# Kernel tuning notes

Measured on AMD Instinct MI355X. Metric: run time of the kernel, lower is better.

The kernel has to match this reference:

```python
import jax, jax.numpy as jnp
import numpy as np

TEMPERATURE = 0.1
THR = 0.2
BORDER_RM = 2


def setup_inputs() -> dict:
    key = jax.random.key(0)
    k0, k1 = jax.random.split(key)
    N, L, S, C = 2, 4800, 4800, 256
    return {
        "feat_c0": jax.random.normal(k0, (N, L, C), dtype=jnp.float32),
        "feat_c1": jax.random.normal(k1, (N, S, C), dtype=jnp.float32),
        "h0c": 60, "w0c": 80, "h1c": 60, "w1c": 80,
    }


def _border_valid(h, w, bd):
    # Faithful to torch mask_border: only the FIRST `bd` rows/cols are masked
    # (the negative slices m[:, -bd:0] in the source are empty no-ops).
    vh = jnp.arange(h) >= bd
    vw = jnp.arange(w) >= bd
    return (vh[:, None] & vw[None, :]).reshape(-1)  # [h*w]


def reference(feat_c0, feat_c1, h0c, w0c, h1c, w1c):
    C = feat_c0.shape[-1]
    scale = 1.0 / (C ** 0.5)  # 'sqrt_feat_dim' feature normalizer
    f0 = feat_c0 * scale
    f1 = feat_c1 * scale

    # dual-softmax confidence matrix [N, L, S]
    sim = jnp.einsum("nlc,nsc->nls", f0, f1) / TEMPERATURE
    conf = jax.nn.softmax(sim, axis=1) * jax.nn.softmax(sim, axis=2)

    # threshold + border removal (no padding masks in data)
    mask = conf > THR
    valid0 = _border_valid(h0c, w0c, BORDER_RM)  # [L]
    valid1 = _border_valid(h1c, w1c, BORDER_RM)  # [S]
    mask = mask & valid0[None, :, None] & valid1[None, None, :]

    # mutual nearest neighbour filtering
    mask = mask & (conf == conf.max(axis=2, keepdims=True)) \
                & (conf == conf.max(axis=1, keepdims=True))

    # match extraction (JIT-friendly padded form):
    # j_ids[b, i] = column of the (unique) True in row i; match_mask marks valid rows.
    j_ids = jnp.argmax(mask, axis=2)               # [N, L] int
    match_mask = jnp.any(mask, axis=2)             # [N, L] bool
    mconf = jnp.take_along_axis(conf, j_ids[..., None], axis=2)[..., 0]
    mconf = jnp.where(match_mask, mconf, 0.0)      # [N, L]

    return conf, match_mask, j_ids, mconf
```

## Files before the change

### kernel.cpp

```cpp
#include <hip/hip_runtime.h>


#define Ncst 2
#define Lc 4800
#define Sc 4800
#define Cc 256
#define KA 512
#define KB 256
#define LP 4864
#define THRC 0.2f

typedef float f32x4 __attribute__((ext_vector_type(4)));
typedef _Float16 f16x8 __attribute__((ext_vector_type(8)));
typedef _Float16 f16x4 __attribute__((ext_vector_type(4)));

#define AS1(p) ((__attribute__((address_space(1))) void*)(p))
#define AS3(p) ((__attribute__((address_space(3))) void*)(p))

__global__ __launch_bounds__(256) void convert_kernel(
    const float* __restrict__ f0, const float* __restrict__ f1,
    unsigned short* __restrict__ A2, unsigned short* __restrict__ B2,
    float* __restrict__ rs, float* __restrict__ cs)
{
    int idx = blockIdx.x * 256 + threadIdx.x;
    if (idx < Ncst * Lc) { rs[idx] = 0.f; cs[idx] = 0.f; }
    if (idx >= Ncst * LP * (Cc / 8)) return;
    int k8  = idx & (Cc / 8 - 1);
    int row = (idx >> 5) % LP;
    int n   = idx / (LP * (Cc / 8));

    float av[8], bv[8];
    if (row < Lc) {
        const float4* pa = (const float4*)(f0 + ((size_t)n * Lc + row) * Cc + k8 * 8);
        float4 a0 = pa[0], a1 = pa[1];
        av[0]=a0.x; av[1]=a0.y; av[2]=a0.z; av[3]=a0.w;
        av[4]=a1.x; av[5]=a1.y; av[6]=a1.z; av[7]=a1.w;
        const float4* pb = (const float4*)(f1 + ((size_t)n * Sc + row) * Cc + k8 * 8);
        float4 b0 = pb[0], b1 = pb[1];
        bv[0]=b0.x; bv[1]=b0.y; bv[2]=b0.z; bv[3]=b0.w;
        bv[4]=b1.x; bv[5]=b1.y; bv[6]=b1.z; bv[7]=b1.w;
    } else {
        for (int i = 0; i < 8; ++i) { av[i] = 0.f; bv[i] = 0.f; }
    }

    _Float16 ahi[8], alo[8], bhi[8];
#pragma unroll
    for (int i = 0; i < 8; ++i) {
        _Float16 h = (_Float16)av[i];
        ahi[i] = h;
        alo[i] = (_Float16)(av[i] - (float)h);
        bhi[i] = (_Float16)bv[i];
    }
    size_t abase = ((size_t)n * LP + row) * KA + k8 * 8;
    size_t bbase = ((size_t)n * LP + row) * KB + k8 * 8;
    *(uint4*)&A2[abase]       = *(uint4*)ahi;
    *(uint4*)&A2[abase + 256] = *(uint4*)alo;
    *(uint4*)&B2[bbase]       = *(uint4*)bhi;
}

template <int DUMMY>
__global__ __launch_bounds__(256, 3) void gemm_kernel(
    const unsigned short* __restrict__ A2, const unsigned short* __restrict__ B2,
    _Float16* __restrict__ eout, float* __restrict__ rs, float* __restrict__ cs)
{
    __shared__ __attribute__((aligned(16))) unsigned short lds[2][1536 * 8];

    int flat = blockIdx.x + 38 * blockIdx.y + 1444 * blockIdx.z;
    int m    = (flat & 7) * 361 + (flat >> 3);
    const int tn = m % 38;
    const int tm = (m / 38) % 38;
    const int n  = m / 1444;

    const int tid  = threadIdx.x;
    const int wave = tid >> 6;
    const int lane = tid & 63;
    const int wm   = wave >> 1;
    const int wn   = wave & 1;
    const int ml   = lane & 15;
    const int kq   = lane >> 4;

    const unsigned short* Ab = A2 + ((size_t)n * LP + (size_t)tm * 128) * KA;
    const unsigned short* Bb = B2 + ((size_t)n * LP + (size_t)tn * 128) * KB;

    const unsigned short* gsrc[6];
    int gdst[6];
#pragma unroll
    for (int c = 0; c < 6; ++c) {
        int reg = c >> 1;
        int s   = (c & 1) * 256 + tid;
        int row = s >> 2;
        int q   = (s & 3) ^ ((row >> 1) & 3);
        if (reg == 0)      gsrc[c] = Ab + (size_t)row * KA + q * 8;
        else if (reg == 1) gsrc[c] = Ab + (size_t)row * KA + 256 + q * 8;
        else               gsrc[c] = Bb + (size_t)row * KB + q * 8;
        gdst[c] = (reg * 512 + s) * 8;
    }

    int aoff[4], boff[4];
#pragma unroll
    for (int i = 0; i < 4; ++i) {
        int ar = wm * 64 + i * 16 + ml;
        aoff[i] = (ar * 4 + (kq ^ ((ar >> 1) & 3))) * 8;
        int br = wn * 64 + i * 16 + ml;
        boff[i] = (br * 4 + (kq ^ ((br >> 1) & 3))) * 8;
    }

#define STAGE(bb, tt) do { _Pragma("unroll") for (int c_ = 0; c_ < 6; ++c_) \
    __builtin_amdgcn_global_load_lds(AS1(gsrc[c_] + (tt) * 32), AS3(&lds[bb][gdst[c_]]), 16, 0, 0); } while (0)

    f32x4 acc[4][4] = {};

    STAGE(0, 0);
    __syncthreads();

#pragma unroll
    for (int t = 0; t < 8; ++t) {
        const int b = t & 1;
        if (t < 7) STAGE(b ^ 1, t + 1);
        f16x8 ah[4], al[4], bf_[4];
#pragma unroll
        for (int i = 0; i < 4; ++i) {
            ah[i]  = *(const f16x8*)&lds[b][aoff[i]];
            al[i]  = *(const f16x8*)&lds[b][4096 + aoff[i]];
            bf_[i] = *(const f16x8*)&lds[b][8192 + boff[i]];
        }
#pragma unroll
        for (int i = 0; i < 4; ++i)
#pragma unroll
            for (int j = 0; j < 4; ++j) {
                acc[i][j] = __builtin_amdgcn_mfma_f32_16x16x32_f16(ah[i], bf_[j], acc[i][j], 0, 0, 0);
                acc[i][j] = __builtin_amdgcn_mfma_f32_16x16x32_f16(al[i], bf_[j], acc[i][j], 0, 0, 0);
            }
        __syncthreads();
    }
#undef STAGE

    const float alpha = 5.0f / 128.0f;
#pragma unroll
    for (int i = 0; i < 4; ++i)
#pragma unroll
        for (int r = 0; r < 4; ++r) {
            int gl = tm * 128 + wm * 64 + i * 16 + kq * 4 + r;
            bool rok = gl < Lc;
#pragma unroll
            for (int j = 0; j < 4; ++j) {
                int gs = tn * 128 + wn * 64 + j * 16 + ml;
                bool ok = rok && (gs < Sc);
                acc[i][j][r] = ok ? __expf(acc[i][j][r] * alpha) : 0.f;
            }
        }
#pragma unroll
    for (int i = 0; i < 4; ++i)
#pragma unroll
        for (int r = 0; r < 4; ++r) {
            float rp = acc[i][0][r] + acc[i][1][r] + acc[i][2][r] + acc[i][3][r];
            rp += __shfl_xor(rp, 1);
            rp += __shfl_xor(rp, 2);
            rp += __shfl_xor(rp, 4);
            rp += __shfl_xor(rp, 8);
            int gl = tm * 128 + wm * 64 + i * 16 + kq * 4 + r;
            if (ml == 0 && gl < Lc) atomicAdd(&rs[(size_t)n * Lc + gl], rp);
        }
#pragma unroll
    for (int j = 0; j < 4; ++j) {
        float cp = 0.f;
#pragma unroll
        for (int i = 0; i < 4; ++i)
#pragma unroll
            for (int r = 0; r < 4; ++r) cp += acc[i][j][r];
        cp += __shfl_xor(cp, 16);
        cp += __shfl_xor(cp, 32);
        int gs = tn * 128 + wn * 64 + j * 16 + ml;
        if (kq == 0 && gs < Sc) atomicAdd(&cs[(size_t)n * Sc + gs], cp);
    }

    float* tb = (float*)&lds[0][0];
    const int CS = 132;
#pragma unroll
    for (int p = 0; p < 2; ++p) {
        __syncthreads();
#pragma unroll
        for (int ih = 0; ih < 2; ++ih) {
            int i   = 2 * p + ih;
            int lr0 = wm * 32 + ih * 16 + kq * 4;
#pragma unroll
            for (int j = 0; j < 4; ++j) {
                int col = wn * 64 + j * 16 + ml;
#pragma unroll
                for (int r = 0; r < 4; ++r)
                    tb[(lr0 + r) * CS + col] = acc[i][j][r];
            }
        }
        __syncthreads();
#pragma unroll
        for (int u = 0; u < 8; ++u) {
            int idx = u * 256 + tid;
            int lr  = idx >> 5;
            int cv  = idx & 31;
            int grow = tm * 128 + (lr >> 5) * 64 + (2 * p + ((lr >> 4) & 1)) * 16 + (lr & 15);
            int gcol = tn * 128 + cv * 4;
            if (grow < Lc && gcol + 3 < Sc) {
                f32x4 v = *(const f32x4*)&tb[lr * CS + cv * 4];
                f16x4 h;
                h.x = (_Float16)v.x; h.y = (_Float16)v.y;
                h.z = (_Float16)v.z; h.w = (_Float16)v.w;
                *(f16x4*)&eout[((size_t)n * Lc + grow) * Sc + gcol] = h;
            }
        }
    }
}

__global__ __launch_bounds__(256) void conf_kernel(
    const _Float16* __restrict__ E, float* __restrict__ conf,
    const float* __restrict__ rs, const float* __restrict__ cs,
    float* __restrict__ rcm)
{
    __shared__ float sw[4];
    int b = blockIdx.x;
    int n = b / Lc;
    const f16x8* erow = (const f16x8*)(E + (size_t)b * Sc);
    f32x4* crow = (f32x4*)(conf + (size_t)b * Sc);
    const f32x4* csv = (const f32x4*)(cs + (size_t)n * Sc);
    int tid = threadIdx.x;
    float riv = 1.0f / rs[b];
    float lmax = 0.f;
    for (int v = tid; v < Sc / 8; v += 256) {
        f16x8 e8 = erow[v];
        f32x4 ca = csv[2 * v], cb = csv[2 * v + 1];
        f32x4 o0, o1;
        o0.x = (float)e8[0]; o0.y = (float)e8[1]; o0.z = (float)e8[2]; o0.w = (float)e8[3];
        o1.x = (float)e8[4]; o1.y = (float)e8[5]; o1.z = (float)e8[6]; o1.w = (float)e8[7];
        f32x4 ia, ib;
        ia.x = 1.0f / ca.x; ia.y = 1.0f / ca.y; ia.z = 1.0f / ca.z; ia.w = 1.0f / ca.w;
        ib.x = 1.0f / cb.x; ib.y = 1.0f / cb.y; ib.z = 1.0f / cb.z; ib.w = 1.0f / cb.w;
        o0 = o0 * o0 * riv * ia;
        o1 = o1 * o1 * riv * ib;
        __builtin_nontemporal_store(o0, &crow[2 * v]);
        __builtin_nontemporal_store(o1, &crow[2 * v + 1]);
        lmax = fmaxf(lmax, fmaxf(fmaxf(o0.x, o0.y), fmaxf(o0.z, o0.w)));
        lmax = fmaxf(lmax, fmaxf(fmaxf(o1.x, o1.y), fmaxf(o1.z, o1.w)));
    }
#pragma unroll
    for (int off = 1; off < 64; off <<= 1) lmax = fmaxf(lmax, __shfl_xor(lmax, off));
    if ((tid & 63) == 0) sw[tid >> 6] = lmax;
    __syncthreads();
    if (tid == 0) rcm[b] = fmaxf(fmaxf(sw[0], sw[1]), fmaxf(sw[2], sw[3]));
}

__global__ __launch_bounds__(256) void finalize_kernel(
    const float* __restrict__ conf, const float* __restrict__ rcm,
    const int* __restrict__ h0p, const int* __restrict__ w0p,
    const int* __restrict__ h1p, const int* __restrict__ w1p,
    float* __restrict__ out_match, float* __restrict__ out_j, float* __restrict__ out_mconf)
{
    int i = blockIdx.x * 256 + threadIdx.x;
    if (i >= Ncst * Lc) return;
    int n = i / Lc, l = i % Lc;
    float mm = rcm[i];
    float fm = 0.f, fj = 0.f, fc = 0.f;
    if (mm > THRC) {
        int w0 = *w0p, w1 = *w1p;
        if ((l / w0) >= 2 && (l % w0) >= 2) {
            const float* rowp = conf + ((size_t)n * Lc + l) * Sc;
            for (int s = 0; s < Sc; ++s) {
                float c = rowp[s];
                if (c == mm && (s / w1) >= 2 && (s % w1) >= 2) {
                    bool ismax = true;
                    const float* colp = conf + (size_t)n * Lc * Sc + s;
                    for (int lp = 0; lp < Lc; ++lp) {
                        if (colp[(size_t)lp * Sc] > c) { ismax = false; break; }
                    }
                    if (ismax) { fm = 1.f; fj = (float)s; fc = c; break; }
                }
            }
        }
    }
    out_match[i] = fm; out_j[i] = fj; out_mconf[i] = fc;
}

extern "C" void kernel_launch(void* const* d_in, const int* in_sizes, int n_in,
                              void* d_out, int out_size, void* d_ws, size_t ws_size,
                              hipStream_t stream) {
    const float* f0 = (const float*)d_in[0];
    const float* f1 = (const float*)d_in[1];
    const int* h0p = (const int*)d_in[2];
    const int* w0p = (const int*)d_in[3];
    const int* h1p = (const int*)d_in[4];
    const int* w1p = (const int*)d_in[5];

    char* ws = (char*)d_ws;
    unsigned short* A2 = (unsigned short*)ws;
    unsigned short* B2 = (unsigned short*)(ws + 9961472);
    _Float16* E = (_Float16*)(ws + 14942208);
    float* rs  = (float*)(ws + 107102208);
    float* cs  = (float*)(ws + 107140608);
    float* rcm = (float*)(ws + 107179008);

    float* conf      = (float*)d_out;
    float* out_match = conf + (size_t)Ncst * Lc * Sc;
    float* out_j     = out_match + Ncst * Lc;
    float* out_mconf = out_j + Ncst * Lc;

    convert_kernel<<<(Ncst * LP * (Cc / 8) + 255) / 256, 256, 0, stream>>>(
        f0, f1, A2, B2, rs, cs);

    dim3 gg(38, 38, Ncst);
    gemm_kernel<0><<<gg, 256, 0, stream>>>(A2, B2, E, rs, cs);

    conf_kernel<<<Ncst * Lc, 256, 0, stream>>>(E, conf, rs, cs, rcm);

    finalize_kernel<<<(Ncst * Lc + 255) / 256, 256, 0, stream>>>(
        conf, rcm, h0p, w0p, h1p, w1p, out_match, out_j, out_mconf);
}
```

Baseline: 312.9 us.

## Drop split-fp16 low term in GEMM and use one wave per conf row

Removes the hi/lo fp16 compensation of feat_c0, so the GEMM does a single fp16 MFMA pass with half the A staging and smaller LDS, and occupancy rises to 4 blocks. The epilogue stages fp16 values in LDS and writes 8-wide vectors. conf_kernel now processes one row per wave without block-level reduction. Accuracy of the similarity drops, which could flip near-tie mutual-NN or threshold decisions.

```diff
diff --git a/kernel.cpp b/kernel.cpp
--- a/kernel.cpp
+++ b/kernel.cpp
@@ -5,14 +5,11 @@
 #define Lc 4800
 #define Sc 4800
 #define Cc 256
-#define KA 512
-#define KB 256
 #define LP 4864
 #define THRC 0.2f
 
 typedef float f32x4 __attribute__((ext_vector_type(4)));
 typedef _Float16 f16x8 __attribute__((ext_vector_type(8)));
-typedef _Float16 f16x4 __attribute__((ext_vector_type(4)));
 
 #define AS1(p) ((__attribute__((address_space(1))) void*)(p))
 #define AS3(p) ((__attribute__((address_space(3))) void*)(p))
@@ -28,6 +25,7 @@
     int k8  = idx & (Cc / 8 - 1);
     int row = (idx >> 5) % LP;
     int n   = idx / (LP * (Cc / 8));
+    size_t dst = ((size_t)n * LP + row) * Cc + k8 * 8;
 
     float av[8], bv[8];
     if (row < Lc) {
@@ -43,27 +41,19 @@
         for (int i = 0; i < 8; ++i) { av[i] = 0.f; bv[i] = 0.f; }
     }
 
-    _Float16 ahi[8], alo[8], bhi[8];
-#pragma unroll
-    for (int i = 0; i < 8; ++i) {
-        _Float16 h = (_Float16)av[i];
-        ahi[i] = h;
-        alo[i] = (_Float16)(av[i] - (float)h);
-        bhi[i] = (_Float16)bv[i];
-    }
-    size_t abase = ((size_t)n * LP + row) * KA + k8 * 8;
-    size_t bbase = ((size_t)n * LP + row) * KB + k8 * 8;
-    *(uint4*)&A2[abase]       = *(uint4*)ahi;
-    *(uint4*)&A2[abase + 256] = *(uint4*)alo;
-    *(uint4*)&B2[bbase]       = *(uint4*)bhi;
+    _Float16 ah[8], bh[8];
+#pragma unroll
+    for (int i = 0; i < 8; ++i) { ah[i] = (_Float16)av[i]; bh[i] = (_Float16)bv[i]; }
+    *(uint4*)&A2[dst] = *(uint4*)ah;
+    *(uint4*)&B2[dst] = *(uint4*)bh;
 }
 
 template <int DUMMY>
-__global__ __launch_bounds__(256, 3) void gemm_kernel(
+__global__ __launch_bounds__(256, 4) void gemm_kernel(
     const unsigned short* __restrict__ A2, const unsigned short* __restrict__ B2,
     _Float16* __restrict__ eout, float* __restrict__ rs, float* __restrict__ cs)
 {
-    __shared__ __attribute__((aligned(16))) unsigned short lds[2][1536 * 8];
+    __shared__ __attribute__((aligned(16))) unsigned short lds[2][1024 * 8];
 
     int flat = blockIdx.x + 38 * blockIdx.y + 1444 * blockIdx.z;
     int m    = (flat & 7) * 361 + (flat >> 3);
@@ -79,21 +69,18 @@
     const int ml   = lane & 15;
     const int kq   = lane >> 4;
 
-    const unsigned short* Ab = A2 + ((size_t)n * LP + (size_t)tm * 128) * KA;
-    const unsigned short* Bb = B2 + ((size_t)n * LP + (size_t)tn * 128) * KB;
-
-    const unsigned short* gsrc[6];
-    int gdst[6];
-#pragma unroll
-    for (int c = 0; c < 6; ++c) {
-        int reg = c >> 1;
+    const unsigned short* Ab = A2 + ((size_t)n * LP + (size_t)tm * 128) * Cc;
+    const unsigned short* Bb = B2 + ((size_t)n * LP + (size_t)tn * 128) * Cc;
+
+    const unsigned short* gsrc[4];
+    int gdst[4];
+#pragma unroll
+    for (int c = 0; c < 4; ++c) {
         int s   = (c & 1) * 256 + tid;
         int row = s >> 2;
         int q   = (s & 3) ^ ((row >> 1) & 3);
-        if (reg == 0)      gsrc[c] = Ab + (size_t)row * KA + q * 8;
-        else if (reg == 1) gsrc[c] = Ab + (size_t)row * KA + 256 + q * 8;
-        else               gsrc[c] = Bb + (size_t)row * KB + q * 8;
-        gdst[c] = (reg * 512 + s) * 8;
+        gsrc[c] = ((c < 2) ? Ab : Bb) + (size_t)row * Cc + q * 8;
+        gdst[c] = (((c < 2) ? 0 : 512) + s) * 8;
     }
 
     int aoff[4], boff[4];
@@ -105,7 +92,7 @@
         boff[i] = (br * 4 + (kq ^ ((br >> 1) & 3))) * 8;
     }
 
-#define STAGE(bb, tt) do { _Pragma("unroll") for (int c_ = 0; c_ < 6; ++c_) \
+#define STAGE(bb, tt) do { _Pragma("unroll") for (int c_ = 0; c_ < 4; ++c_) \
     __builtin_amdgcn_global_load_lds(AS1(gsrc[c_] + (tt) * 32), AS3(&lds[bb][gdst[c_]]), 16, 0, 0); } while (0)
 
     f32x4 acc[4][4] = {};
@@ -117,20 +104,17 @@
     for (int t = 0; t < 8; ++t) {
         const int b = t & 1;
         if (t < 7) STAGE(b ^ 1, t + 1);
-        f16x8 ah[4], al[4], bf_[4];
+        f16x8 af[4], bf_[4];
 #pragma unroll
         for (int i = 0; i < 4; ++i) {
-            ah[i]  = *(const f16x8*)&lds[b][aoff[i]];
-            al[i]  = *(const f16x8*)&lds[b][4096 + aoff[i]];
-            bf_[i] = *(const f16x8*)&lds[b][8192 + boff[i]];
+            af[i]  = *(const f16x8*)&lds[b][aoff[i]];
+            bf_[i] = *(const f16x8*)&lds[b][4096 + boff[i]];
         }
 #pragma unroll
         for (int i = 0; i < 4; ++i)
 #pragma unroll
-            for (int j = 0; j < 4; ++j) {
-                acc[i][j] = __builtin_amdgcn_mfma_f32_16x16x32_f16(ah[i], bf_[j], acc[i][j], 0, 0, 0);
-                acc[i][j] = __builtin_amdgcn_mfma_f32_16x16x32_f16(al[i], bf_[j], acc[i][j], 0, 0, 0);
-            }
+            for (int j = 0; j < 4; ++j)
+                acc[i][j] = __builtin_amdgcn_mfma_f32_16x16x32_f16(af[i], bf_[j], acc[i][j], 0, 0, 0);
         __syncthreads();
     }
 #undef STAGE
@@ -174,7 +158,7 @@
         if (kq == 0 && gs < Sc) atomicAdd(&cs[(size_t)n * Sc + gs], cp);
     }
 
-    float* tb = (float*)&lds[0][0];
+    _Float16* tb = (_Float16*)&lds[0][0];
     const int CS = 132;
 #pragma unroll
     for (int p = 0; p < 2; ++p) {
@@ -188,23 +172,20 @@
                 int col = wn * 64 + j * 16 + ml;
 #pragma unroll
                 for (int r = 0; r < 4; ++r)
-                    tb[(lr0 + r) * CS + col] = acc[i][j][r];
+                    tb[(lr0 + r) * CS + col] = (_Float16)acc[i][j][r];
             }
         }
         __syncthreads();
 #pragma unroll
-        for (int u = 0; u < 8; ++u) {
+        for (int u = 0; u < 4; ++u) {
             int idx = u * 256 + tid;
-            int lr  = idx >> 5;
-            int cv  = idx & 31;
+            int lr  = idx >> 4;
+            int cv  = idx & 15;
             int grow = tm * 128 + (lr >> 5) * 64 + (2 * p + ((lr >> 4) & 1)) * 16 + (lr & 15);
-            int gcol = tn * 128 + cv * 4;
-            if (grow < Lc && gcol + 3 < Sc) {
-                f32x4 v = *(const f32x4*)&tb[lr * CS + cv * 4];
-                f16x4 h;
-                h.x = (_Float16)v.x; h.y = (_Float16)v.y;
-                h.z = (_Float16)v.z; h.w = (_Float16)v.w;
-                *(f16x4*)&eout[((size_t)n * Lc + grow) * Sc + gcol] = h;
+            int gcol = tn * 128 + cv * 8;
+            if (grow < Lc && gcol + 7 < Sc) {
+                f16x8 h = *(const f16x8*)&tb[lr * CS + cv * 8];
+                *(f16x8*)&eout[((size_t)n * Lc + grow) * Sc + gcol] = h;
             }
         }
     }
@@ -215,36 +196,37 @@
     const float* __restrict__ rs, const float* __restrict__ cs,
     float* __restrict__ rcm)
 {
-    __shared__ float sw[4];
-    int b = blockIdx.x;
-    int n = b / Lc;
-    const f16x8* erow = (const f16x8*)(E + (size_t)b * Sc);
-    f32x4* crow = (f32x4*)(conf + (size_t)b * Sc);
+    int w = blockIdx.x * 4 + (threadIdx.x >> 6);
+    int lane = threadIdx.x & 63;
+    int n = w / Lc;
+    const f16x8* erow = (const f16x8*)(E + (size_t)w * Sc);
+    f32x4* crow = (f32x4*)(conf + (size_t)w * Sc);
     const f32x4* csv = (const f32x4*)(cs + (size_t)n * Sc);
-    int tid = threadIdx.x;
-    float riv = 1.0f / rs[b];
+    float riv = 1.0f / rs[w];
     float lmax = 0.f;
-    for (int v = tid; v < Sc / 8; v += 256) {
-        f16x8 e8 = erow[v];
-        f32x4 ca = csv[2 * v], cb = csv[2 * v + 1];
-        f32x4 o0, o1;
-        o0.x = (float)e8[0]; o0.y = (float)e8[1]; o0.z = (float)e8[2]; o0.w = (float)e8[3];
-        o1.x = (float)e8[4]; o1.y = (float)e8[5]; o1.z = (float)e8[6]; o1.w = (float)e8[7];
-        f32x4 ia, ib;
-        ia.x = 1.0f / ca.x; ia.y = 1.0f / ca.y; ia.z = 1.0f / ca.z; ia.w = 1.0f / ca.w;
-        ib.x = 1.0f / cb.x; ib.y = 1.0f / cb.y; ib.z = 1.0f / cb.z; ib.w = 1.0f / cb.w;
-        o0 = o0 * o0 * riv * ia;
-        o1 = o1 * o1 * riv * ib;
-        __builtin_nontemporal_store(o0, &crow[2 * v]);
-        __builtin_nontemporal_store(o1, &crow[2 * v + 1]);
-        lmax = fmaxf(lmax, fmaxf(fmaxf(o0.x, o0.y), fmaxf(o0.z, o0.w)));
-        lmax = fmaxf(lmax, fmaxf(fmaxf(o1.x, o1.y), fmaxf(o1.z, o1.w)));
+#pragma unroll
+    for (int u = 0; u < 10; ++u) {
+        int v = u * 64 + lane;
+        if (v < Sc / 8) {
+            f16x8 e8 = erow[v];
+            f32x4 ca = csv[2 * v], cb = csv[2 * v + 1];
+            f32x4 o0, o1;
+            o0.x = (float)e8[0]; o0.y = (float)e8[1]; o0.z = (float)e8[2]; o0.w = (float)e8[3];
+            o1.x = (float)e8[4]; o1.y = (float)e8[5]; o1.z = (float)e8[6]; o1.w = (float)e8[7];
+            f32x4 ia, ib;
+            ia.x = 1.0f / ca.x; ia.y = 1.0f / ca.y; ia.z = 1.0f / ca.z; ia.w = 1.0f / ca.w;
+            ib.x = 1.0f / cb.x; ib.y = 1.0f / cb.y; ib.z = 1.0f / cb.z; ib.w = 1.0f / cb.w;
+            o0 = o0 * o0 * riv * ia;
+            o1 = o1 * o1 * riv * ib;
+            __builtin_nontemporal_store(o0, &crow[2 * v]);
+            __builtin_nontemporal_store(o1, &crow[2 * v + 1]);
+            lmax = fmaxf(lmax, fmaxf(fmaxf(o0.x, o0.y), fmaxf(o0.z, o0.w)));
+            lmax = fmaxf(lmax, fmaxf(fmaxf(o1.x, o1.y), fmaxf(o1.z, o1.w)));
+        }
     }
 #pragma unroll
     for (int off = 1; off < 64; off <<= 1) lmax = fmaxf(lmax, __shfl_xor(lmax, off));
-    if ((tid & 63) == 0) sw[tid >> 6] = lmax;
-    __syncthreads();
-    if (tid == 0) rcm[b] = fmaxf(fmaxf(sw[0], sw[1]), fmaxf(sw[2], sw[3]));
+    if (lane == 0) rcm[w] = lmax;
 }
 
 __global__ __launch_bounds__(256) void finalize_kernel(
@@ -290,11 +272,11 @@
 
     char* ws = (char*)d_ws;
     unsigned short* A2 = (unsigned short*)ws;
-    unsigned short* B2 = (unsigned short*)(ws + 9961472);
-    _Float16* E = (_Float16*)(ws + 14942208);
-    float* rs  = (float*)(ws + 107102208);
-    float* cs  = (float*)(ws + 107140608);
-    float* rcm = (float*)(ws + 107179008);
+    unsigned short* B2 = (unsigned short*)(ws + 4980736);
+    _Float16* E = (_Float16*)(ws + 9961472);
+    float* rs  = (float*)(ws + 102121472);
+    float* cs  = (float*)(ws + 102159872);
+    float* rcm = (float*)(ws + 102198272);
 
     float* conf      = (float*)d_out;
     float* out_match = conf + (size_t)Ncst * Lc * Sc;
@@ -307,7 +289,7 @@
     dim3 gg(38, 38, Ncst);
     gemm_kernel<0><<<gg, 256, 0, stream>>>(A2, B2, E, rs, cs);
 
-    conf_kernel<<<Ncst * Lc, 256, 0, stream>>>(E, conf, rs, cs, rcm);
+    conf_kernel<<<Ncst * Lc / 4, 256, 0, stream>>>(E, conf, rs, cs, rcm);
 
     finalize_kernel<<<(Ncst * Lc + 255) / 256, 256, 0, stream>>>(
         conf, rcm, h0p, w0p, h1p, w1p, out_match, out_j, out_mconf);
```

Result: no change. 307.0 us (-1.9%).
